# Kernel optimization log

Hardware: AMD Instinct MI355X
Metric: run time of the kernel (lower is better)

Reference implementation:

```python
import jax, jax.numpy as jnp
import numpy as np

# NOTE: SoftAttn (not shown in source) is assumed to be a channel-wise softmax over the
# kernel_size**2 attention maps, as is standard in involution/dynamic-conv designs.

def conv2d(x, w, b=None, stride=1, pad=0, dil=1):
    y = jax.lax.conv_general_dilated(
        x, w, (stride, stride), [(pad, pad), (pad, pad)],
        rhs_dilation=(dil, dil), dimension_numbers=('NCHW', 'OIHW', 'NCHW'))
    return y if b is None else y + b[None, :, None, None]

def prelu(x, a):
    return jnp.where(x >= 0, x, a * x)

def pixel_shuffle(x, r):
    b, c, h, w = x.shape
    x = x.reshape(b, c // (r * r), r, r, h, w)
    x = x.transpose(0, 1, 4, 2, 5, 3)  # b, c', h, r, w, r
    return x.reshape(b, c // (r * r), h * r, w * r)

def aflb(x, aw, ab, fw):
    # Adaptive Fine-grained Local Block: per-position attention over k^2 taps,
    # broadcast across input channels, then contracted with the conv weight.
    k = 3
    C = x.shape[1]
    att = jax.nn.softmax(conv2d(x, aw, ab, pad=1), axis=1)  # [b, k*k, H, W]
    # unfold (channel-major, spatial-minor, matching torch F.unfold)
    p = jax.lax.conv_general_dilated_patches(
        x, (k, k), (1, 1), [(1, 1), (1, 1)],
        dimension_numbers=('NCHW', 'OIHW', 'NCHW'))  # [b, C*k*k, H, W]
    b_, _, H, W = p.shape
    p = p.reshape(b_, C, k * k, H, W)
    atx = p * att[:, None]  # broadcast attention over channels
    return jnp.einsum('bcphw,ocp->bohw', atx, fw.reshape(fw.shape[0], C, k * k))

def rmrs(x, wa, ba, wb, bb, wc, bc, awA, abA, fwA, awB, abB, fwB):
    o = jnp.concatenate([
        conv2d(x, wa, ba, pad=1),
        conv2d(x, wb, bb, pad=2, dil=2),
        conv2d(x, wc, bc, pad=3, dil=3)], axis=1)
    o = aflb(o, awA, abA, fwA)
    o = aflb(o, awB, abB, fwB)
    return jax.nn.relu(o + x)


def setup_inputs() -> dict:
    key = jax.random.key(0)
    ks = iter(jax.random.split(key, 64))
    def rn(shape, s=0.05):
        return jax.random.normal(next(ks), shape, jnp.float32) * s
    a = lambda: jnp.full((1,), 0.25, jnp.float32)
    d = dict(
        ms_up=rn((2, 4, 256, 256), 1.0),
        ms_org=rn((2, 4, 64, 64), 1.0),
        pan=rn((2, 1, 256, 256), 1.0),
        w_up4=rn((64, 4, 3, 3)), b_up4=jnp.zeros(64, jnp.float32), a_up4=a(),
        w_blk53=rn((30, 5, 3, 3)), b_blk53=jnp.zeros(30, jnp.float32), a_blk53=a(),
        w_blk43=rn((30, 4, 3, 3)), b_blk43=jnp.zeros(30, jnp.float32), a_blk43=a(),
        w1a=rn((20, 60, 3, 3)), b1a=jnp.zeros(20, jnp.float32),
        w1b=rn((20, 60, 3, 3)), b1b=jnp.zeros(20, jnp.float32),
        w1c=rn((20, 60, 3, 3)), b1c=jnp.zeros(20, jnp.float32),
        aw1=rn((9, 60, 3, 3)), ab1=jnp.zeros(9, jnp.float32), fw1=rn((60, 60, 3, 3)),
        aw2=rn((9, 60, 3, 3)), ab2=jnp.zeros(9, jnp.float32), fw2=rn((60, 60, 3, 3)),
        w_blk2=rn((30, 60, 3, 3)), b_blk2=jnp.zeros(30, jnp.float32), a_blk2=a(),
        w2a=rn((10, 30, 3, 3)), b2a=jnp.zeros(10, jnp.float32),
        w2b=rn((10, 30, 3, 3)), b2b=jnp.zeros(10, jnp.float32),
        w2c=rn((10, 30, 3, 3)), b2c=jnp.zeros(10, jnp.float32),
        aw3=rn((9, 30, 3, 3)), ab3=jnp.zeros(9, jnp.float32), fw3=rn((30, 30, 3, 3)),
        aw4=rn((9, 30, 3, 3)), ab4=jnp.zeros(9, jnp.float32), fw4=rn((30, 30, 3, 3)),
        w_c6=rn((4, 30, 3, 3)), b_c6=jnp.zeros(4, jnp.float32),
    )
    return d


def reference(ms_up, ms_org, pan,
              w_up4, b_up4, a_up4,
              w_blk53, b_blk53, a_blk53,
              w_blk43, b_blk43, a_blk43,
              w1a, b1a, w1b, b1b, w1c, b1c,
              aw1, ab1, fw1, aw2, ab2, fw2,
              w_blk2, b_blk2, a_blk2,
              w2a, b2a, w2b, b2b, w2c, b2c,
              aw3, ab3, fw3, aw4, ab4, fw4,
              w_c6, b_c6):
    ms_org_up = prelu(pixel_shuffle(conv2d(ms_org, w_up4, b_up4, pad=1), 4), a_up4)
    data1 = jnp.concatenate([ms_org_up, pan], axis=1)  # [b,5,H,W]
    pan_conv = prelu(conv2d(data1, w_blk53, b_blk53, pad=1), a_blk53)
    ms_up_conv = prelu(conv2d(ms_up, w_blk43, b_blk43, pad=1), a_blk43)
    out1 = jnp.concatenate([ms_up_conv, pan_conv], axis=1)  # [b,60,H,W]
    out2 = rmrs(out1, w1a, b1a, w1b, b1b, w1c, b1c, aw1, ab1, fw1, aw2, ab2, fw2)
    out3 = prelu(conv2d(out2, w_blk2, b_blk2, pad=1), a_blk2)  # [b,30,H,W]
    out3 = rmrs(out3, w2a, b2a, w2b, b2b, w2c, b2c, aw3, ab3, fw3, aw4, ab4, fw4)
    out8 = conv2d(out3, w_c6, b_c6, pad=1)
    return out8 + ms_up
```

## Files before the change

kernel.cpp:

```cpp
#include <hip/hip_runtime.h>

typedef __attribute__((ext_vector_type(8))) short short8;
typedef __attribute__((ext_vector_type(4))) float f32x4;
typedef __attribute__((ext_vector_type(4))) int i32x4;

#define HW 65536

__device__ __forceinline__ float bf2f(unsigned short u){
    union { unsigned int i; float f; } x; x.i = ((unsigned int)u) << 16; return x.f;
}
__device__ __forceinline__ unsigned short f2bf(float f){
    union { float f; unsigned int i; } x; x.f = f;
    unsigned int r = x.i + 0x7fffu + ((x.i >> 16) & 1u);
    return (unsigned short)(r >> 16);
}
__device__ __forceinline__ unsigned int pack2(float a, float b){
    return (unsigned int)f2bf(a) | ((unsigned int)f2bf(b) << 16);
}
__device__ __forceinline__ i32x4 addrelu4(i32x4 a, i32x4 b){
    i32x4 o;
#pragma unroll
    for (int k = 0; k < 4; ++k) {
        unsigned int ua = (unsigned int)a[k], ub = (unsigned int)b[k];
        float x0 = bf2f((unsigned short)(ua & 0xffff)) + bf2f((unsigned short)(ub & 0xffff));
        float x1 = bf2f((unsigned short)(ua >> 16))    + bf2f((unsigned short)(ub >> 16));
        o[k] = (int)(((unsigned int)f2bf(fmaxf(x0, 0.f))) |
                     ((unsigned int)f2bf(fmaxf(x1, 0.f)) << 16));
    }
    return o;
}

template<int PRELU>
__global__ __launch_bounds__(256, 4) void sconv2_k(
    const unsigned short* __restrict__ inA, const unsigned short* __restrict__ wfA,
    const float* __restrict__ biasA, const float* __restrict__ alA, int coffA,
    const unsigned short* __restrict__ inB, const unsigned short* __restrict__ wfB,
    const float* __restrict__ biasB, const float* __restrict__ alB, int coffB,
    unsigned short* __restrict__ outb, int cpad)
{
    constexpr int CPIN = 32, SGR = 4, SGRP = 5, SPX = 66;
    constexpr int NSTGDW = 3 * SPX * SGRP * 4;
    constexpr int ODP = 20;
    constexpr int OUTOFF = NSTGDW;
    __shared__ __align__(16) unsigned int sm[NSTGDW + 64 * ODP];
    const int tid = threadIdx.x;
    const int lane = tid & 63, wv = tid >> 6;
    const int col = lane & 15, g = lane >> 4;
    const int bx = blockIdx.x;
    const int xcd = bx & 7, t = bx >> 3;
    const int y0 = xcd * 32 + (t & 31);
    const int x0 = ((t >> 5) & 3) * 64;
    const int which = blockIdx.z >> 1, b = blockIdx.z & 1;
    const unsigned short* in = which ? inB : inA;
    const unsigned short* wfrag = which ? wfB : wfA;
    const float* bias = which ? biasB : biasA;
    const float* alphap = which ? alB : alA;
    const int coff = which ? coffB : coffA;
    const unsigned short* inb = in + (size_t)b * HW * CPIN;

#pragma unroll
    for (int rr = 0; rr < 3; ++rr) {
        const int yy = y0 + rr - 1;
        for (int u = tid; u < SPX * SGR; u += 256) {
            const int slot = u & (SGR - 1), px = u / SGR;
            const int xx = x0 - 1 + px;
            i32x4 v = {0,0,0,0};
            if ((unsigned)yy < 256u && (unsigned)xx < 256u)
                v = *(const i32x4*)(inb + (size_t)(yy * 256 + xx) * CPIN + slot * 8);
            *(i32x4*)&sm[((rr * SPX + px) * SGRP + slot) * 4] = v;
        }
    }
    if (tid < 64) sm[OUTOFF + tid * ODP + 15] = 0;
    __syncthreads();

    const short8* wp = (const short8*)wfrag;
    f32x4 acc[2][2];
#pragma unroll
    for (int mt = 0; mt < 2; ++mt)
#pragma unroll
        for (int c = 0; c < 2; ++c) acc[mt][c] = (f32x4){0.f,0.f,0.f,0.f};
#pragma unroll
    for (int tap = 0; tap < 9; ++tap) {
        const int dy = tap / 3 - 1, dx = tap % 3 - 1;
        const int rl = dy + 1;
        short8 af[2];
#pragma unroll
        for (int mt = 0; mt < 2; ++mt)
            af[mt] = wp[(tap * 2 + mt) * 64 + lane];
        const int pl = 1 + wv * 16 + col + dx;
        const int c2 = tap & 1;
        short8 bf = *(const short8*)&sm[((rl * SPX + pl) * SGRP + g) * 4];
#pragma unroll
        for (int mt = 0; mt < 2; ++mt)
            acc[mt][c2] = __builtin_amdgcn_mfma_f32_16x16x32_bf16(af[mt], bf, acc[mt][c2], 0, 0, 0);
    }
    const float al = PRELU ? __ldg(alphap) : 0.f;
    const int px = wv * 16 + col;
#pragma unroll
    for (int mt = 0; mt < 2; ++mt) {
        const f32x4 a = acc[mt][0] + acc[mt][1];
#pragma unroll
        for (int e = 0; e < 2; ++e) {
            const int rb = mt * 16 + g * 4 + e * 2;
            if (rb < 30) {
                float v0 = a[e * 2]     + __ldg(bias + rb);
                float v1 = a[e * 2 + 1] + ((rb + 1 < 30) ? __ldg(bias + rb + 1) : 0.f);
                if (PRELU) { v0 = v0 >= 0.f ? v0 : al * v0; v1 = v1 >= 0.f ? v1 : al * v1; }
                if (rb + 1 >= 30) v1 = 0.f;
                sm[OUTOFF + px * ODP + (rb >> 1)] = pack2(v0, v1);
            }
        }
    }
    __syncthreads();
    {
        const int slot = tid & 3, opx = tid >> 2;
        i32x4 v = *(i32x4*)&sm[OUTOFF + opx * ODP + slot * 4];
        const size_t go = ((size_t)b * HW + (size_t)y0 * 256 + x0 + opx) * cpad + coff + slot * 8;
        *(i32x4*)(outb + go) = v;
    }
}

template<int KK, int PRELU>
__global__ __launch_bounds__(256, 4) void sconv_k(
    const unsigned short* __restrict__ in,
    const unsigned short* __restrict__ wfrag,
    const float* __restrict__ bias,
    const float* __restrict__ alphap,
    unsigned short* __restrict__ outb, int cpad, int coff)
{
    constexpr int CPIN = KK * 32, SGR = KK * 4, SGRP = SGR + 1, SPX = 66;
    constexpr int NSTGDW = 3 * SPX * SGRP * 4;
    constexpr int ODP = 20;
    constexpr int OUTOFF = NSTGDW;
    __shared__ __align__(16) unsigned int sm[NSTGDW + 64 * ODP];
    const int tid = threadIdx.x;
    const int lane = tid & 63, wv = tid >> 6;
    const int col = lane & 15, g = lane >> 4;
    const int bx = blockIdx.x;
    const int xcd = bx & 7, t = bx >> 3;
    const int y0 = xcd * 32 + (t & 31);
    const int x0 = ((t >> 5) & 3) * 64;
    const int b = blockIdx.z;
    const unsigned short* inb = in + (size_t)b * HW * CPIN;

#pragma unroll
    for (int rr = 0; rr < 3; ++rr) {
        const int yy = y0 + rr - 1;
        for (int u = tid; u < SPX * SGR; u += 256) {
            const int slot = u & (SGR - 1), px = u / SGR;
            const int xx = x0 - 1 + px;
            i32x4 v = {0,0,0,0};
            if ((unsigned)yy < 256u && (unsigned)xx < 256u)
                v = *(const i32x4*)(inb + (size_t)(yy * 256 + xx) * CPIN + slot * 8);
            *(i32x4*)&sm[((rr * SPX + px) * SGRP + slot) * 4] = v;
        }
    }
    if (tid < 64) sm[OUTOFF + tid * ODP + 15] = 0;
    __syncthreads();

    const short8* wp = (const short8*)wfrag;
    f32x4 acc[2][2];
#pragma unroll
    for (int mt = 0; mt < 2; ++mt)
#pragma unroll
        for (int c = 0; c < 2; ++c) acc[mt][c] = (f32x4){0.f,0.f,0.f,0.f};
#pragma unroll
    for (int tap = 0; tap < 9; ++tap) {
        const int dy = tap / 3 - 1, dx = tap % 3 - 1;
        const int rl = dy + 1;
        short8 af[2][KK];
#pragma unroll
        for (int mt = 0; mt < 2; ++mt)
#pragma unroll
            for (int kk = 0; kk < KK; ++kk)
                af[mt][kk] = wp[((tap * 2 + mt) * KK + kk) * 64 + lane];
        const int pl = 1 + wv * 16 + col + dx;
#pragma unroll
        for (int kk = 0; kk < KK; ++kk) {
            const int c2 = (KK == 2) ? kk : (tap & 1);
            short8 bf = *(const short8*)&sm[((rl * SPX + pl) * SGRP + kk * 4 + g) * 4];
#pragma unroll
            for (int mt = 0; mt < 2; ++mt)
                acc[mt][c2] = __builtin_amdgcn_mfma_f32_16x16x32_bf16(af[mt][kk], bf, acc[mt][c2], 0, 0, 0);
        }
    }
    const float al = PRELU ? __ldg(alphap) : 0.f;
    const int px = wv * 16 + col;
#pragma unroll
    for (int mt = 0; mt < 2; ++mt) {
        const f32x4 a = acc[mt][0] + acc[mt][1];
#pragma unroll
        for (int e = 0; e < 2; ++e) {
            const int rb = mt * 16 + g * 4 + e * 2;
            if (rb < 30) {
                float v0 = a[e * 2]     + __ldg(bias + rb);
                float v1 = a[e * 2 + 1] + ((rb + 1 < 30) ? __ldg(bias + rb + 1) : 0.f);
                if (PRELU) { v0 = v0 >= 0.f ? v0 : al * v0; v1 = v1 >= 0.f ? v1 : al * v1; }
                if (rb + 1 >= 30) v1 = 0.f;
                sm[OUTOFF + px * ODP + (rb >> 1)] = pack2(v0, v1);
            }
        }
    }
    __syncthreads();
    {
        const int slot = tid & 3, opx = tid >> 2;
        i32x4 v = *(i32x4*)&sm[OUTOFF + opx * ODP + slot * 4];
        const size_t go = ((size_t)b * HW + (size_t)y0 * 256 + x0 + opx) * cpad + coff + slot * 8;
        *(i32x4*)(outb + go) = v;
    }
}

template<int KK, int MR>
__global__ __launch_bounds__(384, (KK == 2 ? 5 : 8)) void trident_p(
    const unsigned short* __restrict__ in,
    const unsigned short* __restrict__ wf0, const unsigned short* __restrict__ wf1,
    const unsigned short* __restrict__ wf2,
    const float* __restrict__ b0, const float* __restrict__ b1, const float* __restrict__ b2,
    unsigned short* __restrict__ outb)
{
    constexpr int CPIN = KK * 32, CPAD = KK * 32;
    constexpr int SGR = KK * 4, SGRP = SGR + 1, SPX = 38, SROWS = 8;
    constexpr int MT_ = (KK == 2) ? 2 : 1;
    constexpr int CPP = KK * 4, ODP = (CPP + 1) * 4;
    constexpr int NSTGDW = SROWS * SPX * SGRP * 4;
    __shared__ __align__(16) unsigned int sm[NSTGDW];

    const int tid = threadIdx.x;
    const int lane = tid & 63, wv = tid >> 6;
    const int col = lane & 15, g = lane >> 4;
    const int bx = blockIdx.x;
    const int xcd = bx & 7, t = bx >> 3;
    const int y0 = xcd * 32 + (t & 15) * 2;
    const int x0 = ((t >> 4) & 7) * 32;
    const int b = blockIdx.z;
    const unsigned short* inb = in + (size_t)b * HW * CPIN;

    for (int u = tid; u < SROWS * SPX * SGR; u += 384) {
        const int slot = u & (SGR - 1);
        const int px = (u / SGR) % SPX;
        const int row = u / (SGR * SPX);
        const int yy = y0 + row - 3, xx = x0 - 3 + px;
        i32x4 v = {0,0,0,0};
        if ((unsigned)yy < 256u && (unsigned)xx < 256u)
            v = *(const i32x4*)(inb + (size_t)(yy * 256 + xx) * CPIN + slot * 8);
        *(i32x4*)&sm[((row * SPX + px) * SGRP + slot) * 4] = v;
    }
    __syncthreads();

    const int r = (wv >= 3) ? 1 : 0;
    const int dil = wv - r * 3, d = dil + 1;
    const unsigned short* wfx = (dil == 0) ? wf0 : ((dil == 1) ? wf1 : wf2);
    const float* bs = (dil == 0) ? b0 : ((dil == 1) ? b1 : b2);
    const short8* wp = (const short8*)wfx;

    f32x4 acc[MT_][2][2];
#pragma unroll
    for (int mt = 0; mt < MT_; ++mt)
#pragma unroll
        for (int nf = 0; nf < 2; ++nf)
#pragma unroll
            for (int c = 0; c < 2; ++c) acc[mt][nf][c] = (f32x4){0.f,0.f,0.f,0.f};

#pragma unroll
    for (int tap = 0; tap < 9; ++tap) {
        const int dy = tap / 3 - 1, dx = tap % 3 - 1;
        const int rl = 3 + r + dy * d;
        short8 af[MT_][KK];
#pragma unroll
        for (int mt = 0; mt < MT_; ++mt)
#pragma unroll
            for (int kk = 0; kk < KK; ++kk)
                af[mt][kk] = wp[((tap * MT_ + mt) * KK + kk) * 64 + lane];
#pragma unroll
        for (int nf = 0; nf < 2; ++nf) {
            const int pl = 3 + nf * 16 + col + dx * d;
#pragma unroll
            for (int kk = 0; kk < KK; ++kk) {
                const int c2 = (KK == 2) ? kk : (tap & 1);
                short8 bf = *(const short8*)&sm[((rl * SPX + pl) * SGRP + kk * 4 + g) * 4];
#pragma unroll
                for (int mt = 0; mt < MT_; ++mt)
                    acc[mt][nf][c2] = __builtin_amdgcn_mfma_f32_16x16x32_bf16(af[mt][kk], bf, acc[mt][nf][c2], 0, 0, 0);
            }
        }
    }
    __syncthreads();

#pragma unroll
    for (int nf = 0; nf < 2; ++nf) {
        const int px = nf * 16 + col;
        const int base = (r * 32 + px) * ODP;
#pragma unroll
        for (int mt = 0; mt < MT_; ++mt) {
            const f32x4 a = acc[mt][nf][0] + acc[mt][nf][1];
#pragma unroll
            for (int e = 0; e < 2; ++e) {
                const int rb = mt * 16 + g * 4 + e * 2;
                if (rb < MR) {
                    float v0 = a[e * 2] + __ldg(bs + rb);
                    float v1 = (rb + 1 < MR) ? a[e * 2 + 1] + __ldg(bs + rb + 1) : 0.f;
                    sm[base + ((dil * MR + rb) >> 1)] = pack2(v0, v1);
                }
            }
        }
    }
    {
        constexpr int NPAD = CPP * 4 - 3 * MR / 2;
        if (tid < 64 * NPAD) {
            const int pxr = tid / NPAD, dwp = 3 * MR / 2 + tid % NPAD;
            sm[pxr * ODP + dwp] = 0;
        }
    }
    __syncthreads();

    for (int u = tid; u < 64 * CPP; u += 384) {
        const int slot = u & (CPP - 1), pxr = u / CPP;
        const int rr = pxr >> 5, opx = pxr & 31;
        i32x4 v = *(i32x4*)&sm[pxr * ODP + slot * 4];
        const size_t go = ((size_t)b * HW + (size_t)(y0 + rr) * 256 + x0 + opx) * CPAD + slot * 8;
        *(i32x4*)(outb + go) = v;
    }
}

template<int KK, int RPB, int RES>
__global__ __launch_bounds__(256, 4) void aflb_p(
    const unsigned short* __restrict__ in,
    const unsigned short* __restrict__ awf, const float* __restrict__ ab,
    const unsigned short* __restrict__ fwf,
    const unsigned short* __restrict__ res,
    unsigned short* __restrict__ outb)
{
    constexpr int CPIN = KK * 32, MTT = 2 * KK, CPAD = 16 * MTT;
    constexpr int SROWS = RPB + 2, SPX = 66, SGR = KK * 4, SGRP = SGR + 1;
    constexpr int CPP = CPAD / 8, ODP = (CPP + 1) * 4;
    constexpr int NSTGDW = SROWS * SPX * SGRP * 4;
    constexpr int ATOFF = NSTGDW;
    constexpr int NATT = RPB * 64 * 9;
    constexpr int OUTOFF = ATOFF + NATT;
    __shared__ __align__(16) unsigned int sm[OUTOFF + RPB * 64 * ODP];

    const int tid = threadIdx.x;
    const int lane = tid & 63, wv = tid >> 6;
    const int col = lane & 15, g = lane >> 4;
    const int bx = blockIdx.x;
    const int xcd = bx & 7, t = bx >> 3;
    const int y0 = (RPB == 1) ? (xcd * 32 + (t & 31)) : (xcd * 32 + (t & 15) * 2);
    const int xseg = (RPB == 1) ? ((t >> 5) & 3) : ((t >> 4) & 3);
    const int x0 = xseg * 64;
    const int b = blockIdx.z;
    const unsigned short* inb = in + (size_t)b * HW * CPIN;

    for (int u = tid; u < SROWS * SPX * SGR; u += 256) {
        const int slot = u & (SGR - 1);
        const int px = (u / SGR) % SPX;
        const int row = u / (SGR * SPX);
        const int yy = y0 + row - 1, xx = x0 - 1 + px;
        i32x4 v = {0,0,0,0};
        if ((unsigned)yy < 256u && (unsigned)xx < 256u)
            v = *(const i32x4*)(inb + (size_t)(yy * 256 + xx) * CPIN + slot * 8);
        *(i32x4*)&sm[((row * SPX + px) * SGRP + slot) * 4] = v;
    }
    __syncthreads();

    const short8* awp = (const short8*)awf;
    const short8* fwp = (const short8*)fwf;

    constexpr int NF1 = (RPB == 1) ? 1 : 2;
    const int arow = (RPB == 1) ? 0 : (wv >> 1);
    const int apx0 = (RPB == 1) ? (wv * 16) : ((wv & 1) * 32);
    f32x4 aacc[NF1][2];
#pragma unroll
    for (int nf = 0; nf < NF1; ++nf)
#pragma unroll
        for (int c = 0; c < 2; ++c) aacc[nf][c] = (f32x4){0.f,0.f,0.f,0.f};
#pragma unroll
    for (int tap = 0; tap < 9; ++tap) {
        const int dy = tap / 3 - 1, dx = tap % 3 - 1;
        const int rl = arow + dy + 1;
        short8 afa[KK];
#pragma unroll
        for (int kk = 0; kk < KK; ++kk)
            afa[kk] = awp[(tap * KK + kk) * 64 + lane];
#pragma unroll
        for (int nf = 0; nf < NF1; ++nf) {
            const int pl = 1 + apx0 + nf * 16 + col + dx;
#pragma unroll
            for (int kk = 0; kk < KK; ++kk) {
                const int c2 = (KK == 2) ? kk : (tap & 1);
                short8 bf = *(const short8*)&sm[((rl * SPX + pl) * SGRP + kk * 4 + g) * 4];
                aacc[nf][c2] = __builtin_amdgcn_mfma_f32_16x16x32_bf16(afa[kk], bf, aacc[nf][c2], 0, 0, 0);
            }
        }
    }
#pragma unroll
    for (int nf = 0; nf < NF1; ++nf) {
        const f32x4 aa = aacc[nf][0] + aacc[nf][1];
        float v[4];
        float m = -1e30f;
#pragma unroll
        for (int r = 0; r < 4; ++r) {
            const int row = g * 4 + r;
            v[r] = (row < 9) ? (aa[r] + __ldg(ab + row)) : -1e30f;
            m = fmaxf(m, v[r]);
        }
        m = fmaxf(m, __shfl_xor(m, 16));
        m = fmaxf(m, __shfl_xor(m, 32));
        float e[4]; float s = 0.f;
#pragma unroll
        for (int r = 0; r < 4; ++r) { e[r] = (g * 4 + r < 9) ? __expf(v[r] - m) : 0.f; s += e[r]; }
        s += __shfl_xor(s, 16);
        s += __shfl_xor(s, 32);
        const float inv = 1.f / s;
        const int px = apx0 + nf * 16 + col;
#pragma unroll
        for (int r = 0; r < 4; ++r) {
            const int row = g * 4 + r;
            if (row < 9) sm[ATOFF + (arow * 64 + px) * 9 + row] = __float_as_uint(e[r] * inv);
        }
    }
    __syncthreads();

    const int prow = (RPB == 1) ? 0 : (wv >> 1);
    const int mth  = (RPB == 1) ? (wv >> 1) : 0;
    const int nfh  = wv & 1;
    f32x4 acc[2][2];
#pragma unroll
    for (int mtl = 0; mtl < 2; ++mtl)
#pragma unroll
        for (int nf = 0; nf < 2; ++nf) acc[mtl][nf] = (f32x4){0.f,0.f,0.f,0.f};
#pragma unroll
    for (int tap = 0; tap < 9; ++tap) {
        const int dy = tap / 3 - 1, dx = tap % 3 - 1;
        const int rl = prow + dy + 1;
        float av[2];
#pragma unroll
        for (int nf = 0; nf < 2; ++nf)
            av[nf] = __uint_as_float(sm[ATOFF + (prow * 64 + nfh * 32 + nf * 16 + col) * 9 + tap]);
        short8 af[2][KK];
#pragma unroll
        for (int mtl = 0; mtl < 2; ++mtl)
#pragma unroll
            for (int kk = 0; kk < KK; ++kk)
                af[mtl][kk] = fwp[((tap * MTT + (RPB == 1 ? mth * 2 + mtl : mtl)) * KK + kk) * 64 + lane];
#pragma unroll
        for (int nf = 0; nf < 2; ++nf) {
            const int pl = 1 + nfh * 32 + nf * 16 + col + dx;
            f32x4 p[2];
            p[0] = (f32x4){0.f,0.f,0.f,0.f}; p[1] = (f32x4){0.f,0.f,0.f,0.f};
#pragma unroll
            for (int kk = 0; kk < KK; ++kk) {
                short8 bf = *(const short8*)&sm[((rl * SPX + pl) * SGRP + kk * 4 + g) * 4];
#pragma unroll
                for (int mtl = 0; mtl < 2; ++mtl)
                    p[mtl] = __builtin_amdgcn_mfma_f32_16x16x32_bf16(af[mtl][kk], bf, p[mtl], 0, 0, 0);
            }
#pragma unroll
            for (int mtl = 0; mtl < 2; ++mtl)
#pragma unroll
                for (int r = 0; r < 4; ++r)
                    acc[mtl][nf][r] = fmaf(av[nf], p[mtl][r], acc[mtl][nf][r]);
        }
    }
    __syncthreads();

#pragma unroll
    for (int mtl = 0; mtl < 2; ++mtl) {
        const int mt = (RPB == 1) ? (mth * 2 + mtl) : mtl;
#pragma unroll
        for (int nf = 0; nf < 2; ++nf) {
            const int px = nfh * 32 + nf * 16 + col;
            const int base = OUTOFF + ((RPB == 2 ? prow * 64 : 0) + px) * ODP;
            const int rp = mt * 8 + g * 2;
            unsigned long long w =
                (unsigned long long)pack2(acc[mtl][nf][0], acc[mtl][nf][1]) |
                ((unsigned long long)pack2(acc[mtl][nf][2], acc[mtl][nf][3]) << 32);
            *(unsigned long long*)&sm[base + rp] = w;
        }
    }
    __syncthreads();

    constexpr int NOUT = RPB * 64 * CPP;
    for (int u = tid; u < NOUT; u += 256) {
        const int slot = u & (CPP - 1);
        const int px = (u / CPP) & 63;
        const int r = (RPB == 2) ? (u / (CPP * 64)) : 0;
        i32x4 v = *(i32x4*)&sm[OUTOFF + ((r * 64 + px) * ODP) + slot * 4];
        const size_t go = ((size_t)b * HW + (size_t)(y0 + r) * 256 + x0 + px) * CPAD + slot * 8;
        if (RES) v = addrelu4(v, *(const i32x4*)(res + go));
        *(i32x4*)(outb + go) = v;
    }
}

__global__ __launch_bounds__(256, 4) void final_k(
    const unsigned short* __restrict__ in,
    const unsigned short* __restrict__ wfrag,
    const float* __restrict__ bias,
    const float* __restrict__ msup, float* __restrict__ outf)
{
    constexpr int CPIN = 32, NF = 2;
    const int lane = threadIdx.x & 63, wv = threadIdx.x >> 6;
    const int col = lane & 15, g = lane >> 4;
    const int bx = blockIdx.x;
    const int xcd = bx & 7, t = bx >> 3;
    const int y = xcd * 32 + (t & 31);
    const int xh = t >> 5;
    const int b = blockIdx.z;
    const int x0 = xh * 128 + wv * 32;

    const unsigned short* inb = in + (size_t)b * HW * CPIN;
    const short8 kz = {0,0,0,0,0,0,0,0};
    const short8* wp = (const short8*)wfrag;

    f32x4 acc[NF];
#pragma unroll
    for (int nf = 0; nf < NF; ++nf) acc[nf] = (f32x4){0.f,0.f,0.f,0.f};
#pragma unroll
    for (int tap = 0; tap < 9; ++tap) {
        const int dy = tap / 3 - 1, dx = tap % 3 - 1;
        const int yy = y + dy;
        const bool yok = (unsigned)yy < 256u;
        const short8 af = wp[tap * 64 + lane];
#pragma unroll
        for (int nf = 0; nf < NF; ++nf) {
            const int xx = x0 + nf * 16 + col + dx;
            const bool ok = yok && ((unsigned)xx < 256u);
            const int pix = ok ? (yy * 256 + xx) : 0;
            short8 bf = *(const short8*)(inb + (size_t)pix * CPIN + g * 8);
            if (!ok) bf = kz;
            acc[nf] = __builtin_amdgcn_mfma_f32_16x16x32_bf16(af, bf, acc[nf], 0, 0, 0);
        }
    }
#pragma unroll
    for (int nf = 0; nf < NF; ++nf) {
        const int pix = y * 256 + x0 + nf * 16 + col;
        if (g == 0) {
#pragma unroll
            for (int r = 0; r < 4; ++r) {
                const size_t oi = ((size_t)b * 4 + r) * HW + pix;
                outf[oi] = acc[nf][r] + __ldg(bias + r) + msup[oi];
            }
        }
    }
}

struct PrepDesc { const float* src; int cout, cin, kksh, mtsh, flags, dstoff, n; };
struct PrepArgs { PrepDesc d[18]; };

__global__ __launch_bounds__(256) void prep_k(PrepArgs pa, unsigned short* __restrict__ wb)
{
    const PrepDesc d = pa.d[blockIdx.y];
    const int e = blockIdx.x * 256 + threadIdx.x;
    if (e >= d.n) return;
    const int j = e & 7;
    const int lane = (e >> 3) & 63;
    const int i512 = e >> 9;
    const int kk = i512 & ((1 << d.kksh) - 1);
    const int mt = (i512 >> d.kksh) & ((1 << d.mtsh) - 1);
    const int tap = i512 >> (d.kksh + d.mtsh);
    const int rpos = mt * 16 + (lane & 15);
    const int kpos = kk * 32 + (lane >> 4) * 8 + j;
    int o = rpos, ic = kpos;
    bool ok = true;
    if (d.flags & 2) {
        if (rpos < 30) o = rpos;
        else if (rpos >= 32 && rpos < 62) o = rpos - 2;
        else ok = false;
    }
    if (d.flags & 1) {
        if (kpos < 30) ic = kpos;
        else if (kpos >= 32 && kpos < 62) ic = kpos - 2;
        else ok = false;
    }
    float v = 0.f;
    if (ok && o < d.cout && ic < d.cin) v = d.src[(o * d.cin + ic) * 9 + tap];
    wb[d.dstoff + e] = f2bf(v);
}

template<int CIN, int COUT, int OCB, int H, int W>
__launch_bounds__(256)
__global__ void upconv_k(const float* __restrict__ in, const float* __restrict__ wgt,
                         const float* __restrict__ bias, float* __restrict__ out)
{
    constexpr int HWp = H * W;
    constexpr int NOCB = COUT / OCB;
    const int tx = threadIdx.x;
    const int lx = tx & 63, ly = tx >> 6;
    const int gx = blockIdx.x * 64 + lx;
    const int gy = blockIdx.y * 4 + ly;
    const int b = blockIdx.z / NOCB;
    const int ocb = blockIdx.z % NOCB;
    const int pixp = gy * W + gx;
    const float* inb = in + (size_t)b * CIN * HWp;

    int off[9]; float mul[9];
#pragma unroll
    for (int dy = 0; dy < 3; ++dy)
#pragma unroll
        for (int dx = 0; dx < 3; ++dx) {
            int p = dy * 3 + dx;
            int yy = gy + dy - 1, xx = gx + dx - 1;
            bool okp = ((unsigned)yy < (unsigned)H) && ((unsigned)xx < (unsigned)W);
            off[p] = okp ? (yy * W + xx) : 0;
            mul[p] = okp ? 1.f : 0.f;
        }
    float acc[OCB];
#pragma unroll
    for (int o = 0; o < OCB; ++o) acc[o] = 0.f;
    const float* wbase = wgt + (size_t)(ocb * OCB) * CIN * 9;
#pragma unroll
    for (int ic = 0; ic < CIN; ++ic) {
        const float* ip = inb + (size_t)ic * HWp;
        float tv[9];
#pragma unroll
        for (int p = 0; p < 9; ++p) tv[p] = __ldg(ip + off[p]) * mul[p];
#pragma unroll
        for (int o = 0; o < OCB; ++o) {
            const float* wq = wbase + (size_t)(o * CIN + ic) * 9;
#pragma unroll
            for (int p = 0; p < 9; ++p) acc[o] = fmaf(tv[p], wq[p], acc[o]);
        }
    }
#pragma unroll
    for (int o = 0; o < OCB; ++o)
        out[((size_t)b * COUT + ocb * OCB + o) * HWp + pixp] = acc[o] + __ldg(bias + ocb * OCB + o);
}

__global__ __launch_bounds__(256) void build_inputs(
    const float* __restrict__ tup, const float* __restrict__ pan,
    const float* __restrict__ aup, const float* __restrict__ msup,
    unsigned short* __restrict__ data1, unsigned short* __restrict__ msb)
{
    const int i = blockIdx.x * 256 + threadIdx.x;
    const int b = i >> 16, pixp = i & 65535;
    const int y = pixp >> 8, x = pixp & 255;
    unsigned short o[32];
#pragma unroll
    for (int c = 0; c < 32; ++c) o[c] = 0;
    unsigned short* dst;
    if (blockIdx.y == 0) {
        const float a = __ldg(aup);
#pragma unroll
        for (int c = 0; c < 4; ++c) {
            const int ch = c * 16 + (y & 3) * 4 + (x & 3);
            float v = tup[(((size_t)b * 64 + ch) << 12) + ((y >> 2) << 6) + (x >> 2)];
            v = (v >= 0.f) ? v : a * v;
            o[c] = f2bf(v);
        }
        o[4] = f2bf(pan[((size_t)b << 16) + pixp]);
        dst = data1;
    } else {
#pragma unroll
        for (int c = 0; c < 4; ++c)
            o[c] = f2bf(msup[(((size_t)b * 4 + c) << 16) + pixp]);
        dst = msb;
    }
    short8* dp = (short8*)(dst + (size_t)i * 32);
#pragma unroll
    for (int q = 0; q < 4; ++q) {
        short8 s;
#pragma unroll
        for (int r = 0; r < 8; ++r) s[r] = (short)o[q * 8 + r];
        dp[q] = s;
    }
}

extern "C" void kernel_launch(void* const* d_in, const int* in_sizes, int n_in,
                              void* d_out, int out_size, void* d_ws, size_t ws_size,
                              hipStream_t stream) {
    const float* ms_up  = (const float*)d_in[0];
    const float* ms_org = (const float*)d_in[1];
    const float* pan    = (const float*)d_in[2];
    const float* w_up4  = (const float*)d_in[3];
    const float* b_up4  = (const float*)d_in[4];
    const float* a_up4  = (const float*)d_in[5];
    const float* w_blk53= (const float*)d_in[6];
    const float* b_blk53= (const float*)d_in[7];
    const float* a_blk53= (const float*)d_in[8];
    const float* w_blk43= (const float*)d_in[9];
    const float* b_blk43= (const float*)d_in[10];
    const float* a_blk43= (const float*)d_in[11];
    const float* w1a=(const float*)d_in[12]; const float* b1a=(const float*)d_in[13];
    const float* w1b=(const float*)d_in[14]; const float* b1b=(const float*)d_in[15];
    const float* w1c=(const float*)d_in[16]; const float* b1c=(const float*)d_in[17];
    const float* aw1=(const float*)d_in[18]; const float* ab1=(const float*)d_in[19];
    const float* fw1=(const float*)d_in[20];
    const float* aw2=(const float*)d_in[21]; const float* ab2=(const float*)d_in[22];
    const float* fw2=(const float*)d_in[23];
    const float* w_blk2=(const float*)d_in[24]; const float* b_blk2=(const float*)d_in[25]; const float* a_blk2=(const float*)d_in[26];
    const float* w2a=(const float*)d_in[27]; const float* b2a=(const float*)d_in[28];
    const float* w2b=(const float*)d_in[29]; const float* b2b=(const float*)d_in[30];
    const float* w2c=(const float*)d_in[31]; const float* b2c=(const float*)d_in[32];
    const float* aw3=(const float*)d_in[33]; const float* ab3=(const float*)d_in[34];
    const float* fw3=(const float*)d_in[35];
    const float* aw4=(const float*)d_in[36]; const float* ab4=(const float*)d_in[37];
    const float* fw4=(const float*)d_in[38];
    const float* w_c6=(const float*)d_in[39]; const float* b_c6=(const float*)d_in[40];

    float* out = (float*)d_out;
    char* ws = (char*)d_ws;

    const size_t BIG = (size_t)2 * HW * 64 * 2;
    const size_t HALF = BIG / 2;
    unsigned short* bufA = (unsigned short*)(ws);
    unsigned short* bufB = (unsigned short*)(ws + BIG);
    unsigned short* bufC = (unsigned short*)(ws + 2 * BIG);
    unsigned short* data1 = bufC;
    float*          t_up  = (float*)(ws + 2 * BIG + HALF);
    unsigned short* msb   = bufB;
    unsigned short* bufD = bufC;
    unsigned short* bufE = bufB;
    unsigned short* bufF = bufA;
    unsigned short* wb = (unsigned short*)(ws + 3 * BIG);

    if (ws_size < 3 * BIG + 1000000) return;

    PrepArgs pa;
    int off = 0, li = 0;
    auto add = [&](const float* s, int cout, int cin, int mtsh, int kksh, int flags) {
        const int n = 9 << (mtsh + kksh + 9);
        pa.d[li].src = s; pa.d[li].cout = cout; pa.d[li].cin = cin;
        pa.d[li].kksh = kksh; pa.d[li].mtsh = mtsh; pa.d[li].flags = flags;
        pa.d[li].dstoff = off; pa.d[li].n = n;
        int ret = off; off += n; ++li; return ret;
    };
    const int o_blk43 = add(w_blk43, 30, 4, 1, 0, 0);
    const int o_blk53 = add(w_blk53, 30, 5, 1, 0, 0);
    const int o_w1a   = add(w1a, 20, 60, 1, 1, 1);
    const int o_w1b   = add(w1b, 20, 60, 1, 1, 1);
    const int o_w1c   = add(w1c, 20, 60, 1, 1, 1);
    const int o_aw1   = add(aw1,  9, 60, 0, 1, 0);
    const int o_fw1   = add(fw1, 60, 60, 2, 1, 0);
    const int o_aw2   = add(aw2,  9, 60, 0, 1, 0);
    const int o_fw2   = add(fw2, 60, 60, 2, 1, 2);
    const int o_blk2  = add(w_blk2, 30, 60, 1, 1, 1);
    const int o_w2a   = add(w2a, 10, 30, 0, 0, 0);
    const int o_w2b   = add(w2b, 10, 30, 0, 0, 0);
    const int o_w2c   = add(w2c, 10, 30, 0, 0, 0);
    const int o_aw3   = add(aw3,  9, 30, 0, 0, 0);
    const int o_fw3   = add(fw3, 30, 30, 1, 0, 0);
    const int o_aw4   = add(aw4,  9, 30, 0, 0, 0);
    const int o_fw4   = add(fw4, 30, 30, 1, 0, 0);
    const int o_c6    = add(w_c6,  4, 30, 0, 0, 0);

    prep_k<<<dim3(144, 18), 256, 0, stream>>>(pa, wb);

    upconv_k<4, 64, 16, 64, 64><<<dim3(1, 16, 8), 256, 0, stream>>>(ms_org, w_up4, b_up4, t_up);
    build_inputs<<<dim3(512, 2), 256, 0, stream>>>(t_up, pan, a_up4, ms_up, data1, msb);

    const dim3 B256(256), B384(384);
    const dim3 G1(1024, 1, 2);
    const dim3 G2(1024, 1, 4);
    const dim3 GP(1024, 1, 2);
    const dim3 GH(512, 1, 2);

    sconv2_k<1><<<G2,B256,0,stream>>>(msb, wb+o_blk43, b_blk43, a_blk43, 0,
                                      data1, wb+o_blk53, b_blk53, a_blk53, 32,
                                      bufA, 64);

    trident_p<2,20><<<GP,B384,0,stream>>>(bufA, wb+o_w1a, wb+o_w1b, wb+o_w1c, b1a, b1b, b1c, bufB);
    aflb_p<2,1,0><<<G1,B256,0,stream>>>(bufB, wb+o_aw1, ab1, wb+o_fw1, nullptr, bufC);
    aflb_p<2,1,1><<<G1,B256,0,stream>>>(bufC, wb+o_aw2, ab2, wb+o_fw2, bufA,   bufB);

    sconv_k<2,1><<<G1,B256,0,stream>>>(bufB, wb+o_blk2, b_blk2, a_blk2, bufD, 32, 0);

    trident_p<1,10><<<GP,B384,0,stream>>>(bufD, wb+o_w2a, wb+o_w2b, wb+o_w2c, b2a, b2b, b2c, bufE);
    aflb_p<1,2,0><<<GH,B256,0,stream>>>(bufE, wb+o_aw3, ab3, wb+o_fw3, nullptr, bufF);
    aflb_p<1,2,1><<<GH,B256,0,stream>>>(bufF, wb+o_aw4, ab4, wb+o_fw4, bufD,   bufE);

    final_k<<<GH,B256,0,stream>>>(bufE, wb+o_c6, b_c6, ms_up, out);
}
```

Before: 190.1 us.

## Add specialized AFLB kernel with 2x32 pixel tiles for 60-channel stage

```diff
diff --git a/kernel.cpp b/kernel.cpp
--- a/kernel.cpp
+++ b/kernel.cpp
@@ -318,6 +318,155 @@
         const int rr = pxr >> 5, opx = pxr & 31;
         i32x4 v = *(i32x4*)&sm[pxr * ODP + slot * 4];
         const size_t go = ((size_t)b * HW + (size_t)(y0 + rr) * 256 + x0 + opx) * CPAD + slot * 8;
+        *(i32x4*)(outb + go) = v;
+    }
+}
+
+template<int RES>
+__global__ __launch_bounds__(256, 5) void aflb2_k(
+    const unsigned short* __restrict__ in,
+    const unsigned short* __restrict__ awf, const float* __restrict__ ab,
+    const unsigned short* __restrict__ fwf,
+    const unsigned short* __restrict__ res,
+    unsigned short* __restrict__ outb)
+{
+    constexpr int KK = 2, CPIN = 64, MTT = 4, CPAD = 64;
+    constexpr int SROWS = 4, SPX = 34, SGR = 8, SGRP = 9;
+    constexpr int CPP = 8, ODP = (CPP + 1) * 4;
+    constexpr int NSTGDW = SROWS * SPX * SGRP * 4;
+    constexpr int ATOFF = NSTGDW;
+    __shared__ __align__(16) unsigned int sm[ATOFF + 2 * 32 * ODP];
+
+    const int tid = threadIdx.x;
+    const int lane = tid & 63, wv = tid >> 6;
+    const int col = lane & 15, g = lane >> 4;
+    const int bx = blockIdx.x;
+    const int xcd = bx & 7, t = bx >> 3;
+    const int y0 = xcd * 32 + (t & 15) * 2;
+    const int x0 = ((t >> 4) & 7) * 32;
+    const int b = blockIdx.z;
+    const unsigned short* inb = in + (size_t)b * HW * CPIN;
+
+    for (int u = tid; u < SROWS * SPX * SGR; u += 256) {
+        const int slot = u & (SGR - 1);
+        const int px = (u / SGR) % SPX;
+        const int row = u / (SGR * SPX);
+        const int yy = y0 + row - 1, xx = x0 - 1 + px;
+        i32x4 v = {0,0,0,0};
+        if ((unsigned)yy < 256u && (unsigned)xx < 256u)
+            v = *(const i32x4*)(inb + (size_t)(yy * 256 + xx) * CPIN + slot * 8);
+        *(i32x4*)&sm[((row * SPX + px) * SGRP + slot) * 4] = v;
+    }
+    __syncthreads();
+
+    const short8* awp = (const short8*)awf;
+    const short8* fwp = (const short8*)fwf;
+
+    {
+        const int r = wv >> 1, apx0 = (wv & 1) * 16;
+        f32x4 aacc[2];
+        aacc[0] = (f32x4){0.f,0.f,0.f,0.f}; aacc[1] = (f32x4){0.f,0.f,0.f,0.f};
+#pragma unroll
+        for (int tap = 0; tap < 9; ++tap) {
+            const int dy = tap / 3 - 1, dx = tap % 3 - 1;
+            const int rl = r + dy + 1;
+            const int pl = 1 + apx0 + col + dx;
+#pragma unroll
+            for (int kk = 0; kk < KK; ++kk) {
+                short8 afa = awp[(tap * KK + kk) * 64 + lane];
+                short8 bf = *(const short8*)&sm[((rl * SPX + pl) * SGRP + kk * 4 + g) * 4];
+                aacc[kk] = __builtin_amdgcn_mfma_f32_16x16x32_bf16(afa, bf, aacc[kk], 0, 0, 0);
+            }
+        }
+        const f32x4 aa = aacc[0] + aacc[1];
+        float v[4];
+        float m = -1e30f;
+#pragma unroll
+        for (int rr = 0; rr < 4; ++rr) {
+            const int row = g * 4 + rr;
+            v[rr] = (row < 9) ? (aa[rr] + __ldg(ab + row)) : -1e30f;
+            m = fmaxf(m, v[rr]);
+        }
+        m = fmaxf(m, __shfl_xor(m, 16));
+        m = fmaxf(m, __shfl_xor(m, 32));
+        float e[4]; float s = 0.f;
+#pragma unroll
+        for (int rr = 0; rr < 4; ++rr) { e[rr] = (g * 4 + rr < 9) ? __expf(v[rr] - m) : 0.f; s += e[rr]; }
+        s += __shfl_xor(s, 16);
+        s += __shfl_xor(s, 32);
+        const float inv = 1.f / s;
+        const int px = apx0 + col;
+#pragma unroll
+        for (int rr = 0; rr < 4; ++rr) {
+            const int row = g * 4 + rr;
+            if (row < 9) sm[ATOFF + (r * 32 + px) * 9 + row] = __float_as_uint(e[rr] * inv);
+        }
+    }
+    __syncthreads();
+
+    const int r = wv >> 1, mth = wv & 1;
+    f32x4 acc[2][2];
+#pragma unroll
+    for (int mtl = 0; mtl < 2; ++mtl)
+#pragma unroll
+        for (int nf = 0; nf < 2; ++nf) acc[mtl][nf] = (f32x4){0.f,0.f,0.f,0.f};
+#pragma unroll
+    for (int tap = 0; tap < 9; ++tap) {
+        const int dy = tap / 3 - 1, dx = tap % 3 - 1;
+        const int rl = r + dy + 1;
+        float av[2];
+#pragma unroll
+        for (int nf = 0; nf < 2; ++nf)
+            av[nf] = __uint_as_float(sm[ATOFF + (r * 32 + nf * 16 + col) * 9 + tap]);
+        short8 af[2][KK];
+#pragma unroll
+        for (int mtl = 0; mtl < 2; ++mtl)
+#pragma unroll
+            for (int kk = 0; kk < KK; ++kk)
+                af[mtl][kk] = fwp[((tap * MTT + mth * 2 + mtl) * KK + kk) * 64 + lane];
+#pragma unroll
+        for (int nf = 0; nf < 2; ++nf) {
+            const int pl = 1 + nf * 16 + col + dx;
+            f32x4 p[2];
+            p[0] = (f32x4){0.f,0.f,0.f,0.f}; p[1] = (f32x4){0.f,0.f,0.f,0.f};
+#pragma unroll
+            for (int kk = 0; kk < KK; ++kk) {
+                short8 bf = *(const short8*)&sm[((rl * SPX + pl) * SGRP + kk * 4 + g) * 4];
+#pragma unroll
+                for (int mtl = 0; mtl < 2; ++mtl)
+                    p[mtl] = __builtin_amdgcn_mfma_f32_16x16x32_bf16(af[mtl][kk], bf, p[mtl], 0, 0, 0);
+            }
+#pragma unroll
+            for (int mtl = 0; mtl < 2; ++mtl)
+#pragma unroll
+                for (int rr = 0; rr < 4; ++rr)
+                    acc[mtl][nf][rr] = fmaf(av[nf], p[mtl][rr], acc[mtl][nf][rr]);
+        }
+    }
+    __syncthreads();
+
+#pragma unroll
+    for (int mtl = 0; mtl < 2; ++mtl) {
+        const int mt = mth * 2 + mtl;
+#pragma unroll
+        for (int nf = 0; nf < 2; ++nf) {
+            const int px = nf * 16 + col;
+            const int base = ATOFF + (r * 32 + px) * ODP;
+            const int rp = mt * 8 + g * 2;
+            unsigned long long w =
+                (unsigned long long)pack2(acc[mtl][nf][0], acc[mtl][nf][1]) |
+                ((unsigned long long)pack2(acc[mtl][nf][2], acc[mtl][nf][3]) << 32);
+            *(unsigned long long*)&sm[base + rp] = w;
+        }
+    }
+    __syncthreads();
+
+    for (int u = tid; u < 2 * 32 * CPP; u += 256) {
+        const int slot = u & (CPP - 1), pxr = u / CPP;
+        const int rr = pxr >> 5, opx = pxr & 31;
+        i32x4 v = *(i32x4*)&sm[ATOFF + pxr * ODP + slot * 4];
+        const size_t go = ((size_t)b * HW + (size_t)(y0 + rr) * 256 + x0 + opx) * CPAD + slot * 8;
+        if (RES) v = addrelu4(v, *(const i32x4*)(res + go));
         *(i32x4*)(outb + go) = v;
     }
 }
@@ -758,8 +907,8 @@
                                       bufA, 64);
 
     trident_p<2,20><<<GP,B384,0,stream>>>(bufA, wb+o_w1a, wb+o_w1b, wb+o_w1c, b1a, b1b, b1c, bufB);
-    aflb_p<2,1,0><<<G1,B256,0,stream>>>(bufB, wb+o_aw1, ab1, wb+o_fw1, nullptr, bufC);
-    aflb_p<2,1,1><<<G1,B256,0,stream>>>(bufC, wb+o_aw2, ab2, wb+o_fw2, bufA,   bufB);
+    aflb2_k<0><<<GP,B256,0,stream>>>(bufB, wb+o_aw1, ab1, wb+o_fw1, nullptr, bufC);
+    aflb2_k<1><<<GP,B256,0,stream>>>(bufC, wb+o_aw2, ab2, wb+o_fw2, bufA,   bufB);
 
     sconv_k<2,1><<<G1,B256,0,stream>>>(bufB, wb+o_blk2, b_blk2, a_blk2, bufD, 32, 0);
 
```

New measurement: 190.4 us. No clear change (+0.2%).
